# Kernel optimization log

Hardware: AMD Instinct MI355X
Metric: run time of the kernel (lower is better)

## Reference

```python
import jax, jax.numpy as jnp
import numpy as np

N = 500_000
B = 10_000
L = N // B  # 50 tokens per session
H = 128


def setup_inputs() -> dict:
    key = jax.random.key(0)
    ks = jax.random.split(key, 7)
    x = jax.random.normal(ks[0], (N, H), dtype=jnp.float32)
    # sorted segment ids: B sessions of length L (every segment non-empty)
    batch = jnp.repeat(jnp.arange(B, dtype=jnp.int32), L)
    # index of the last element of each session
    last_ixs = jnp.arange(B, dtype=jnp.int32) * L + (L - 1)
    s = 1.0 / np.sqrt(H)
    W1_w = jax.random.uniform(ks[1], (H, H), jnp.float32, -s, s)
    W1_b = jax.random.uniform(ks[2], (H,), jnp.float32, -s, s)
    W2_w = jax.random.uniform(ks[3], (H, H), jnp.float32, -s, s)
    W2_b = jax.random.uniform(ks[4], (H,), jnp.float32, -s, s)
    q_w = jax.random.uniform(ks[5], (1, H), jnp.float32, -s, s)
    q_b = jax.random.uniform(ks[6], (1,), jnp.float32, -s, s)
    return {"x": x, "W1_w": W1_w, "W1_b": W1_b, "W2_w": W2_w, "W2_b": W2_b,
            "q_w": q_w, "q_b": q_b, "batch": batch, "last_ixs": last_ixs,
            "num_segments": B}


def reference(x, W1_w, W1_b, W2_w, W2_b, q_w, q_b, batch, last_ixs, num_segments):
    # v_i = x[last_ixs]; repeat_interleave(v_i, bincount(batch)) == v_i[batch] (batch sorted)
    v_n_repeat = x[last_ixs][batch]                                   # [N, H]
    h = jax.nn.sigmoid(v_n_repeat @ W1_w.T + W1_b + x @ W2_w.T + W2_b)  # [N, H]
    e = (h @ q_w.T + q_b)[:, 0]                                       # [N]
    # segment-wise (per-session) numerically-stable softmax
    m = jax.ops.segment_max(e, batch, num_segments=num_segments)      # [B]
    z = jnp.exp(e - m[batch])                                         # [N]
    denom = jax.ops.segment_sum(z, batch, num_segments=num_segments)  # [B]
    alpha = (z / denom[batch])[:, None]                               # [N, 1]
    # scatter_add pooling of alpha * x over sessions
    s_g = jax.ops.segment_sum(alpha * x, batch, num_segments=num_segments)  # [B, H]
    return s_g
```

## Files before the change

### kernel.cpp

```cpp
#include <hip/hip_runtime.h>

#define H_DIM 128
#define L_SESS 50
#define B_SESS 10000
#define LDSTR 136
#define ESTR 5

typedef __bf16 bf16_t;
typedef __bf16 bf16x8 __attribute__((ext_vector_type(8)));
typedef float f32x4 __attribute__((ext_vector_type(4)));

__global__ __launch_bounds__(256) void cvt_kernel(
    const float* __restrict__ w1, const float* __restrict__ w2,
    const float* __restrict__ w1b, const float* __restrict__ w2bi,
    unsigned short* __restrict__ wout, float* __restrict__ bias12) {
  int i = blockIdx.x * 256 + threadIdx.x;
  float4 v = (i < 4096) ? ((const float4*)w1)[i] : ((const float4*)w2)[i - 4096];
  union { bf16_t h[4]; ushort4 u4; } tmp;
  tmp.h[0] = (bf16_t)v.x; tmp.h[1] = (bf16_t)v.y;
  tmp.h[2] = (bf16_t)v.z; tmp.h[3] = (bf16_t)v.w;
  *(ushort4*)(wout + (size_t)4 * i) = tmp.u4;
  if (i < H_DIM) bias12[i] = w1b[i] + w2bi[i];
}

__global__ __launch_bounds__(256, 8) void sess_attn_kernel(
    const float* __restrict__ x, const unsigned short* __restrict__ Wb,
    const float* __restrict__ bias12, const float* __restrict__ qw,
    const float* __restrict__ qb, float* __restrict__ out) {
  __shared__ __attribute__((aligned(16))) unsigned short Xb[64 * LDSTR];
  __shared__ float epart[64 * ESTR];
  __shared__ float alpha_s[64];

  const int t = threadIdx.x;
  const int b = blockIdx.x;
  const int lane = t & 63, w = t >> 6, q = lane >> 4, c = lane & 15;
  const int n0 = w * 32 + c;
  const int n1 = n0 + 16;

  const float* xs = x + (size_t)b * (L_SESS * H_DIM);
  const float4* xsv = (const float4*)xs;
  const bf16x8* W1v = (const bf16x8*)(Wb);
  const bf16x8* W2v = (const bf16x8*)(Wb + 16384);

  float4 v[6];
#pragma unroll
  for (int j = 0; j < 6; ++j) v[j] = xsv[t + 256 * j];
  float4 v6;
  if (t < 64) v6 = xsv[1536 + t];

  const float bias0 = bias12[n0], bias1 = bias12[n1];
  const float qn0 = qw[n0], qn1 = qw[n1], qbv = qb[0];

#pragma unroll
  for (int j = 0; j < 6; ++j) {
    int i = t + 256 * j;
    int row = i >> 5, col = (i & 31) * 4;
    union { bf16_t h[4]; ushort4 u4; } tmp;
    tmp.h[0] = (bf16_t)v[j].x; tmp.h[1] = (bf16_t)v[j].y;
    tmp.h[2] = (bf16_t)v[j].z; tmp.h[3] = (bf16_t)v[j].w;
    *(ushort4*)&Xb[row * LDSTR + col] = tmp.u4;
  }
  if (t < 64) {
    int i = 1536 + t;
    int row = i >> 5, col = (i & 31) * 4;
    union { bf16_t h[4]; ushort4 u4; } tmp;
    tmp.h[0] = (bf16_t)v6.x; tmp.h[1] = (bf16_t)v6.y;
    tmp.h[2] = (bf16_t)v6.z; tmp.h[3] = (bf16_t)v6.w;
    *(ushort4*)&Xb[row * LDSTR + col] = tmp.u4;
  }
  __syncthreads();

  const f32x4 zero4 = {0.f, 0.f, 0.f, 0.f};

  f32x4 accu0 = zero4, accu1 = zero4;
#pragma unroll
  for (int kt = 0; kt < 4; ++kt) {
    const int ko = kt * 32 + q * 8;
    bf16x8 av = *(const bf16x8*)&Xb[49 * LDSTR + ko];
    accu0 = __builtin_amdgcn_mfma_f32_16x16x32_bf16(
        av, W1v[(n0 * H_DIM + ko) >> 3], accu0, 0, 0, 0);
    accu1 = __builtin_amdgcn_mfma_f32_16x16x32_bf16(
        av, W1v[(n1 * H_DIM + ko) >> 3], accu1, 0, 0, 0);
  }
  const float u0 = accu0[0] + bias0;
  const float u1 = accu1[0] + bias1;

  f32x4 acc[4][2];
#pragma unroll
  for (int mt = 0; mt < 4; ++mt) { acc[mt][0] = zero4; acc[mt][1] = zero4; }
#pragma unroll
  for (int kt = 0; kt < 4; ++kt) {
    const int ko = kt * 32 + q * 8;
    bf16x8 b0 = W2v[(n0 * H_DIM + ko) >> 3];
    bf16x8 b1 = W2v[(n1 * H_DIM + ko) >> 3];
#pragma unroll
    for (int mt = 0; mt < 4; ++mt) {
      bf16x8 a = *(const bf16x8*)&Xb[(mt * 16 + c) * LDSTR + ko];
      acc[mt][0] = __builtin_amdgcn_mfma_f32_16x16x32_bf16(a, b0, acc[mt][0], 0, 0, 0);
      acc[mt][1] = __builtin_amdgcn_mfma_f32_16x16x32_bf16(a, b1, acc[mt][1], 0, 0, 0);
    }
  }

#pragma unroll
  for (int mt = 0; mt < 4; ++mt) {
#pragma unroll
    for (int r = 0; r < 4; ++r) {
      float t0 = acc[mt][0][r] + u0;
      float t1 = acc[mt][1][r] + u1;
      float h0 = 1.0f / (1.0f + __expf(-t0));
      float h1 = 1.0f / (1.0f + __expf(-t1));
      float p = h0 * qn0 + h1 * qn1;
#pragma unroll
      for (int off = 1; off <= 8; off <<= 1) p += __shfl_xor(p, off);
      if (c == 0) epart[(mt * 16 + q * 4 + r) * ESTR + w] = p;
    }
  }
  __syncthreads();

  if (t < 64) {
    float e = qbv;
#pragma unroll
    for (int j = 0; j < 4; ++j) e += epart[t * ESTR + j];
    float val = (t < L_SESS) ? e : -1.0e30f;
    float mx = val;
#pragma unroll
    for (int off = 32; off > 0; off >>= 1) mx = fmaxf(mx, __shfl_xor(mx, off));
    float z = (t < L_SESS) ? __expf(e - mx) : 0.f;
    float d = z;
#pragma unroll
    for (int off = 32; off > 0; off >>= 1) d += __shfl_xor(d, off);
    alpha_s[t] = z / d;
  }
  __syncthreads();

  if (t < H_DIM) {
    float s = 0.f;
#pragma unroll
    for (int m = 0; m < L_SESS; ++m) {
      unsigned short pv = Xb[m * LDSTR + t];
      s += alpha_s[m] * __uint_as_float(((unsigned int)pv) << 16);
    }
    out[(size_t)b * H_DIM + t] = s;
  }
}

extern "C" void kernel_launch(void* const* d_in, const int* in_sizes, int n_in,
                              void* d_out, int out_size, void* d_ws, size_t ws_size,
                              hipStream_t stream) {
  const float* x    = (const float*)d_in[0];
  const float* w1   = (const float*)d_in[1];
  const float* w1b  = (const float*)d_in[2];
  const float* w2   = (const float*)d_in[3];
  const float* w2bi = (const float*)d_in[4];
  const float* qw   = (const float*)d_in[5];
  const float* qb   = (const float*)d_in[6];
  float* out = (float*)d_out;

  unsigned short* Wb = (unsigned short*)d_ws;
  float* bias12 = (float*)((char*)d_ws + 65536);

  cvt_kernel<<<32, 256, 0, stream>>>(w1, w2, w1b, w2bi, Wb, bias12);
  sess_attn_kernel<<<B_SESS, 256, 0, stream>>>(x, Wb, bias12, qw, qb, out);
}
```

Measured before the change: 401.4 us.

## Precompute session U via separate MFMA kernel and persist attention blocks with prefetch

```diff
diff --git a/kernel.cpp b/kernel.cpp
--- a/kernel.cpp
+++ b/kernel.cpp
@@ -3,6 +3,8 @@
 #define H_DIM 128
 #define L_SESS 50
 #define B_SESS 10000
+#define NBLK 1024
+#define NITER 10
 #define LDSTR 136
 #define ESTR 5
 
@@ -11,136 +13,187 @@
 typedef float f32x4 __attribute__((ext_vector_type(4)));
 
 __global__ __launch_bounds__(256) void cvt_kernel(
-    const float* __restrict__ w1, const float* __restrict__ w2,
-    const float* __restrict__ w1b, const float* __restrict__ w2bi,
-    unsigned short* __restrict__ wout, float* __restrict__ bias12) {
+    const float* __restrict__ w2, const float* __restrict__ w1b,
+    const float* __restrict__ w2bi, unsigned short* __restrict__ w2out,
+    float* __restrict__ bias12) {
   int i = blockIdx.x * 256 + threadIdx.x;
-  float4 v = (i < 4096) ? ((const float4*)w1)[i] : ((const float4*)w2)[i - 4096];
+  float4 v = ((const float4*)w2)[i];
   union { bf16_t h[4]; ushort4 u4; } tmp;
   tmp.h[0] = (bf16_t)v.x; tmp.h[1] = (bf16_t)v.y;
   tmp.h[2] = (bf16_t)v.z; tmp.h[3] = (bf16_t)v.w;
-  *(ushort4*)(wout + (size_t)4 * i) = tmp.u4;
+  *(ushort4*)(w2out + (size_t)4 * i) = tmp.u4;
   if (i < H_DIM) bias12[i] = w1b[i] + w2bi[i];
 }
 
-__global__ __launch_bounds__(256, 8) void sess_attn_kernel(
-    const float* __restrict__ x, const unsigned short* __restrict__ Wb,
-    const float* __restrict__ bias12, const float* __restrict__ qw,
+__global__ __launch_bounds__(256) void sess_u_kernel(
+    const float* __restrict__ x, const float* __restrict__ w1,
+    const float* __restrict__ bias12, float* __restrict__ U) {
+  __shared__ __attribute__((aligned(16))) unsigned short W1s[H_DIM * LDSTR];
+  __shared__ __attribute__((aligned(16))) unsigned short Vs[16 * LDSTR];
+  const int t = threadIdx.x;
+  const int s0 = blockIdx.x * 16;
+  for (int i = t; i < 4096; i += 256) {
+    float4 v = ((const float4*)w1)[i];
+    int row = i >> 5, col = (i & 31) * 4;
+    union { bf16_t h[4]; ushort4 u4; } tmp;
+    tmp.h[0] = (bf16_t)v.x; tmp.h[1] = (bf16_t)v.y;
+    tmp.h[2] = (bf16_t)v.z; tmp.h[3] = (bf16_t)v.w;
+    *(ushort4*)&W1s[row * LDSTR + col] = tmp.u4;
+  }
+  for (int i = t; i < 512; i += 256) {
+    int j = i >> 5, col = (i & 31) * 4;
+    float4 v = ((const float4*)(x + ((size_t)(s0 + j) * L_SESS + (L_SESS - 1)) * H_DIM))[i & 31];
+    union { bf16_t h[4]; ushort4 u4; } tmp;
+    tmp.h[0] = (bf16_t)v.x; tmp.h[1] = (bf16_t)v.y;
+    tmp.h[2] = (bf16_t)v.z; tmp.h[3] = (bf16_t)v.w;
+    *(ushort4*)&Vs[j * LDSTR + col] = tmp.u4;
+  }
+  __syncthreads();
+  const int lane = t & 63, w = t >> 6, q = lane >> 4, c = lane & 15;
+  const int n0 = (w * 2) * 16 + c, n1 = (w * 2 + 1) * 16 + c;
+  const f32x4 zero4 = {0.f, 0.f, 0.f, 0.f};
+  f32x4 acc0 = zero4, acc1 = zero4;
+#pragma unroll
+  for (int kt = 0; kt < 4; ++kt) {
+    bf16x8 a  = *(const bf16x8*)&Vs[c * LDSTR + kt * 32 + q * 8];
+    bf16x8 b0 = *(const bf16x8*)&W1s[n0 * LDSTR + kt * 32 + q * 8];
+    bf16x8 b1 = *(const bf16x8*)&W1s[n1 * LDSTR + kt * 32 + q * 8];
+    acc0 = __builtin_amdgcn_mfma_f32_16x16x32_bf16(a, b0, acc0, 0, 0, 0);
+    acc1 = __builtin_amdgcn_mfma_f32_16x16x32_bf16(a, b1, acc1, 0, 0, 0);
+  }
+  float bias0 = bias12[n0], bias1 = bias12[n1];
+#pragma unroll
+  for (int r = 0; r < 4; ++r) {
+    int m = q * 4 + r;
+    U[(size_t)(s0 + m) * H_DIM + n0] = acc0[r] + bias0;
+    U[(size_t)(s0 + m) * H_DIM + n1] = acc1[r] + bias1;
+  }
+}
+
+__global__ __launch_bounds__(256, 4) void sess_attn_kernel(
+    const float* __restrict__ x, const unsigned short* __restrict__ W2b,
+    const float* __restrict__ U, const float* __restrict__ qw,
     const float* __restrict__ qb, float* __restrict__ out) {
   __shared__ __attribute__((aligned(16))) unsigned short Xb[64 * LDSTR];
   __shared__ float epart[64 * ESTR];
   __shared__ float alpha_s[64];
 
   const int t = threadIdx.x;
-  const int b = blockIdx.x;
   const int lane = t & 63, w = t >> 6, q = lane >> 4, c = lane & 15;
-  const int n0 = w * 32 + c;
-  const int n1 = n0 + 16;
-
-  const float* xs = x + (size_t)b * (L_SESS * H_DIM);
-  const float4* xsv = (const float4*)xs;
-  const bf16x8* W1v = (const bf16x8*)(Wb);
-  const bf16x8* W2v = (const bf16x8*)(Wb + 16384);
-
+  const int n0 = w * 32 + c, n1 = n0 + 16;
+
+  const bf16x8* W2v = (const bf16x8*)W2b;
+  bf16x8 bw2[4][2];
+#pragma unroll
+  for (int kt = 0; kt < 4; ++kt) {
+    bw2[kt][0] = W2v[(n0 * H_DIM + kt * 32 + q * 8) >> 3];
+    bw2[kt][1] = W2v[(n1 * H_DIM + kt * 32 + q * 8) >> 3];
+  }
+  const float qn0 = qw[n0], qn1 = qw[n1], qbv = qb[0];
+
+  int s = blockIdx.x;
+  int sc = (s < B_SESS) ? s : (B_SESS - 1);
+  const float4* xv = (const float4*)(x + (size_t)sc * (L_SESS * H_DIM));
   float4 v[6];
 #pragma unroll
-  for (int j = 0; j < 6; ++j) v[j] = xsv[t + 256 * j];
+  for (int j = 0; j < 6; ++j) v[j] = xv[t + 256 * j];
   float4 v6;
-  if (t < 64) v6 = xsv[1536 + t];
-
-  const float bias0 = bias12[n0], bias1 = bias12[n1];
-  const float qn0 = qw[n0], qn1 = qw[n1], qbv = qb[0];
-
-#pragma unroll
-  for (int j = 0; j < 6; ++j) {
-    int i = t + 256 * j;
-    int row = i >> 5, col = (i & 31) * 4;
-    union { bf16_t h[4]; ushort4 u4; } tmp;
-    tmp.h[0] = (bf16_t)v[j].x; tmp.h[1] = (bf16_t)v[j].y;
-    tmp.h[2] = (bf16_t)v[j].z; tmp.h[3] = (bf16_t)v[j].w;
-    *(ushort4*)&Xb[row * LDSTR + col] = tmp.u4;
-  }
-  if (t < 64) {
-    int i = 1536 + t;
-    int row = i >> 5, col = (i & 31) * 4;
-    union { bf16_t h[4]; ushort4 u4; } tmp;
-    tmp.h[0] = (bf16_t)v6.x; tmp.h[1] = (bf16_t)v6.y;
-    tmp.h[2] = (bf16_t)v6.z; tmp.h[3] = (bf16_t)v6.w;
-    *(ushort4*)&Xb[row * LDSTR + col] = tmp.u4;
-  }
-  __syncthreads();
+  if (t < 64) v6 = xv[1536 + t];
+  float unx0 = U[(size_t)sc * H_DIM + n0];
+  float unx1 = U[(size_t)sc * H_DIM + n1];
 
   const f32x4 zero4 = {0.f, 0.f, 0.f, 0.f};
 
-  f32x4 accu0 = zero4, accu1 = zero4;
-#pragma unroll
-  for (int kt = 0; kt < 4; ++kt) {
-    const int ko = kt * 32 + q * 8;
-    bf16x8 av = *(const bf16x8*)&Xb[49 * LDSTR + ko];
-    accu0 = __builtin_amdgcn_mfma_f32_16x16x32_bf16(
-        av, W1v[(n0 * H_DIM + ko) >> 3], accu0, 0, 0, 0);
-    accu1 = __builtin_amdgcn_mfma_f32_16x16x32_bf16(
-        av, W1v[(n1 * H_DIM + ko) >> 3], accu1, 0, 0, 0);
-  }
-  const float u0 = accu0[0] + bias0;
-  const float u1 = accu1[0] + bias1;
-
-  f32x4 acc[4][2];
-#pragma unroll
-  for (int mt = 0; mt < 4; ++mt) { acc[mt][0] = zero4; acc[mt][1] = zero4; }
-#pragma unroll
-  for (int kt = 0; kt < 4; ++kt) {
-    const int ko = kt * 32 + q * 8;
-    bf16x8 b0 = W2v[(n0 * H_DIM + ko) >> 3];
-    bf16x8 b1 = W2v[(n1 * H_DIM + ko) >> 3];
+  for (int it = 0; it < NITER; ++it) {
+    __syncthreads();
+    const float u0 = unx0, u1 = unx1;
+
+#pragma unroll
+    for (int j = 0; j < 6; ++j) {
+      int i = t + 256 * j;
+      int row = i >> 5, col = (i & 31) * 4;
+      union { bf16_t h[4]; ushort4 u4; } tmp;
+      tmp.h[0] = (bf16_t)v[j].x; tmp.h[1] = (bf16_t)v[j].y;
+      tmp.h[2] = (bf16_t)v[j].z; tmp.h[3] = (bf16_t)v[j].w;
+      *(ushort4*)&Xb[row * LDSTR + col] = tmp.u4;
+    }
+    if (t < 64) {
+      int i = 1536 + t;
+      int row = i >> 5, col = (i & 31) * 4;
+      union { bf16_t h[4]; ushort4 u4; } tmp;
+      tmp.h[0] = (bf16_t)v6.x; tmp.h[1] = (bf16_t)v6.y;
+      tmp.h[2] = (bf16_t)v6.z; tmp.h[3] = (bf16_t)v6.w;
+      *(ushort4*)&Xb[row * LDSTR + col] = tmp.u4;
+    }
+    __syncthreads();
+
+    if (it + 1 < NITER) {
+      int sn = s + NBLK;
+      int snc = (sn < B_SESS) ? sn : (B_SESS - 1);
+      const float4* xn = (const float4*)(x + (size_t)snc * (L_SESS * H_DIM));
+#pragma unroll
+      for (int j = 0; j < 6; ++j) v[j] = xn[t + 256 * j];
+      if (t < 64) v6 = xn[1536 + t];
+      unx0 = U[(size_t)snc * H_DIM + n0];
+      unx1 = U[(size_t)snc * H_DIM + n1];
+    }
+
+    f32x4 acc[4][2];
+#pragma unroll
+    for (int mt = 0; mt < 4; ++mt) { acc[mt][0] = zero4; acc[mt][1] = zero4; }
+#pragma unroll
+    for (int kt = 0; kt < 4; ++kt) {
+      const int ko = kt * 32 + q * 8;
+#pragma unroll
+      for (int mt = 0; mt < 4; ++mt) {
+        bf16x8 a = *(const bf16x8*)&Xb[(mt * 16 + c) * LDSTR + ko];
+        acc[mt][0] = __builtin_amdgcn_mfma_f32_16x16x32_bf16(a, bw2[kt][0], acc[mt][0], 0, 0, 0);
+        acc[mt][1] = __builtin_amdgcn_mfma_f32_16x16x32_bf16(a, bw2[kt][1], acc[mt][1], 0, 0, 0);
+      }
+    }
+
 #pragma unroll
     for (int mt = 0; mt < 4; ++mt) {
-      bf16x8 a = *(const bf16x8*)&Xb[(mt * 16 + c) * LDSTR + ko];
-      acc[mt][0] = __builtin_amdgcn_mfma_f32_16x16x32_bf16(a, b0, acc[mt][0], 0, 0, 0);
-      acc[mt][1] = __builtin_amdgcn_mfma_f32_16x16x32_bf16(a, b1, acc[mt][1], 0, 0, 0);
-    }
-  }
-
-#pragma unroll
-  for (int mt = 0; mt < 4; ++mt) {
-#pragma unroll
-    for (int r = 0; r < 4; ++r) {
-      float t0 = acc[mt][0][r] + u0;
-      float t1 = acc[mt][1][r] + u1;
-      float h0 = 1.0f / (1.0f + __expf(-t0));
-      float h1 = 1.0f / (1.0f + __expf(-t1));
-      float p = h0 * qn0 + h1 * qn1;
-#pragma unroll
-      for (int off = 1; off <= 8; off <<= 1) p += __shfl_xor(p, off);
-      if (c == 0) epart[(mt * 16 + q * 4 + r) * ESTR + w] = p;
-    }
-  }
-  __syncthreads();
-
-  if (t < 64) {
-    float e = qbv;
-#pragma unroll
-    for (int j = 0; j < 4; ++j) e += epart[t * ESTR + j];
-    float val = (t < L_SESS) ? e : -1.0e30f;
-    float mx = val;
-#pragma unroll
-    for (int off = 32; off > 0; off >>= 1) mx = fmaxf(mx, __shfl_xor(mx, off));
-    float z = (t < L_SESS) ? __expf(e - mx) : 0.f;
-    float d = z;
-#pragma unroll
-    for (int off = 32; off > 0; off >>= 1) d += __shfl_xor(d, off);
-    alpha_s[t] = z / d;
-  }
-  __syncthreads();
-
-  if (t < H_DIM) {
-    float s = 0.f;
-#pragma unroll
-    for (int m = 0; m < L_SESS; ++m) {
-      unsigned short pv = Xb[m * LDSTR + t];
-      s += alpha_s[m] * __uint_as_float(((unsigned int)pv) << 16);
-    }
-    out[(size_t)b * H_DIM + t] = s;
+#pragma unroll
+      for (int r = 0; r < 4; ++r) {
+        float t0 = acc[mt][0][r] + u0;
+        float t1 = acc[mt][1][r] + u1;
+        float h0 = 1.0f / (1.0f + __expf(-t0));
+        float h1 = 1.0f / (1.0f + __expf(-t1));
+        float p = h0 * qn0 + h1 * qn1;
+#pragma unroll
+        for (int off = 1; off <= 8; off <<= 1) p += __shfl_xor(p, off);
+        if (c == 0) epart[(mt * 16 + q * 4 + r) * ESTR + w] = p;
+      }
+    }
+    __syncthreads();
+
+    if (t < 64) {
+      float e = qbv;
+#pragma unroll
+      for (int j = 0; j < 4; ++j) e += epart[t * ESTR + j];
+      float val = (t < L_SESS) ? e : -1.0e30f;
+      float mx = val;
+#pragma unroll
+      for (int off = 32; off > 0; off >>= 1) mx = fmaxf(mx, __shfl_xor(mx, off));
+      float z = (t < L_SESS) ? __expf(e - mx) : 0.f;
+      float d = z;
+#pragma unroll
+      for (int off = 32; off > 0; off >>= 1) d += __shfl_xor(d, off);
+      alpha_s[t] = z / d;
+    }
+    __syncthreads();
+
+    if (t < H_DIM) {
+      float acc_p = 0.f;
+#pragma unroll
+      for (int m = 0; m < L_SESS; ++m) {
+        unsigned short pv = Xb[m * LDSTR + t];
+        acc_p += alpha_s[m] * __uint_as_float(((unsigned int)pv) << 16);
+      }
+      if (s < B_SESS) out[(size_t)s * H_DIM + t] = acc_p;
+    }
+    s += NBLK;
   }
 }
 
@@ -156,9 +209,11 @@
   const float* qb   = (const float*)d_in[6];
   float* out = (float*)d_out;
 
-  unsigned short* Wb = (unsigned short*)d_ws;
-  float* bias12 = (float*)((char*)d_ws + 65536);
-
-  cvt_kernel<<<32, 256, 0, stream>>>(w1, w2, w1b, w2bi, Wb, bias12);
-  sess_attn_kernel<<<B_SESS, 256, 0, stream>>>(x, Wb, bias12, qw, qb, out);
-}
+  unsigned short* W2bf = (unsigned short*)d_ws;
+  float* bias12 = (float*)((char*)d_ws + 32768);
+  float* U = (float*)((char*)d_ws + 36864);
+
+  cvt_kernel<<<16, 256, 0, stream>>>(w2, w1b, w2bi, W2bf, bias12);
+  sess_u_kernel<<<B_SESS / 16, 256, 0, stream>>>(x, w1, bias12, U);
+  sess_attn_kernel<<<NBLK, 256, 0, stream>>>(x, W2bf, U, qw, qb, out);
+}
```

Result: no change. 393.7 us (-1.9%).
